# Optimization experiments

Hardware: AMD Instinct MI355X
Metric: run time of the kernel (lower is better)

## Reference

```python
import jax, jax.numpy as jnp
import numpy as np

NUM_Q_HEADS = 32
NUM_KV_GROUPS = 8
HEAD_SIZE = 128
ROPE_THETA = 10000.0


def _rope_cos_sin(T, dim, dtype=jnp.float32):
    # freqs_cis = polar(1, outer(m, 1/theta^(2i/dim)))
    freqs = 1.0 / (ROPE_THETA ** (jnp.arange(0, dim, 2, dtype=jnp.float32) / dim))
    angle = jnp.arange(T, dtype=jnp.float32)[:, None] * freqs[None, :]  # [T, dim/2]
    return jnp.cos(angle).astype(dtype), jnp.sin(angle).astype(dtype)


def _apply_rope(x, cos, sin):
    # x: [B, H, T, D]; adjacent pairs (x[2i], x[2i+1]) form complex numbers
    xr = x[..., 0::2]
    xi = x[..., 1::2]
    or_ = xr * cos - xi * sin
    oi_ = xr * sin + xi * cos
    # interleave back: (..., D/2, 2) -> (..., D)
    out = jnp.stack([or_, oi_], axis=-1)
    return out.reshape(x.shape)


def setup_inputs() -> dict:
    key = jax.random.key(0)
    ks = jax.random.split(key, 5)
    B, T, C = 2, 1024, 4096
    H, G, D = NUM_Q_HEADS, NUM_KV_GROUPS, HEAD_SIZE
    s = 1.0 / np.sqrt(C)
    return {
        "x": jax.random.normal(ks[0], (B, T, C), dtype=jnp.float32),
        "Wq": jax.random.normal(ks[1], (C, H * D), dtype=jnp.float32) * s,
        "Wk": jax.random.normal(ks[2], (C, G * D), dtype=jnp.float32) * s,
        "Wv": jax.random.normal(ks[3], (C, G * D), dtype=jnp.float32) * s,
        "Wo": jax.random.normal(ks[4], (H * D, C), dtype=jnp.float32) * (1.0 / np.sqrt(H * D)),
        "bo": jnp.zeros((C,), dtype=jnp.float32),
    }


def reference(x, Wq, Wk, Wv, Wo, bo):
    B, T, C = x.shape
    H, G, D = NUM_Q_HEADS, NUM_KV_GROUPS, HEAD_SIZE
    rep = H // G

    q = (x @ Wq).reshape(B, T, H, D).transpose(0, 2, 1, 3)  # [B,H,T,D]
    k = (x @ Wk).reshape(B, T, G, D).transpose(0, 2, 1, 3)  # [B,G,T,D]
    v = (x @ Wv).reshape(B, T, G, D).transpose(0, 2, 1, 3)  # [B,G,T,D]

    cos, sin = _rope_cos_sin(T, D)  # [T, D/2]
    q = _apply_rope(q, cos, sin)
    k = _apply_rope(k, cos, sin)

    # GQA: head h uses group h // rep -> reshape instead of repeat_interleave
    qg = q.reshape(B, G, rep, T, D)
    scores = jnp.einsum("bgrtd,bgsd->bgrts", qg, k) * (D ** -0.5)  # [B,G,rep,T,T]

    causal = jnp.tril(jnp.ones((T, T), dtype=bool))
    scores = jnp.where(causal, scores, -jnp.inf)
    probs = jax.nn.softmax(scores, axis=-1)

    out = jnp.einsum("bgrts,bgsd->bgrtd", probs, v)  # [B,G,rep,T,D]
    out = out.reshape(B, H, T, D).transpose(0, 2, 1, 3).reshape(B, T, H * D)
    return out @ Wo + bo
```

## Files before the change

kernel.cpp:

```cpp
#include <hip/hip_runtime.h>
#include <math.h>
#include <cstdint>
#include <cstddef>

typedef __bf16 bf16_t;
typedef __bf16 bf16x8 __attribute__((ext_vector_type(8)));
typedef __bf16 bf16x4 __attribute__((ext_vector_type(4)));
typedef float f32x4 __attribute__((ext_vector_type(4)));
typedef float f32x16 __attribute__((ext_vector_type(16)));

#define MFMA16(a, b, c) __builtin_amdgcn_mfma_f32_16x16x32_bf16(a, b, c, 0, 0, 0)
#define MFMA32(a, b, c) __builtin_amdgcn_mfma_f32_32x32x16_bf16(a, b, c, 0, 0, 0)

__device__ __forceinline__ void stage16(const void* g, void* l) {
  __builtin_amdgcn_global_load_lds(
      (const __attribute__((address_space(1))) unsigned int*)g,
      (__attribute__((address_space(3))) unsigned int*)l, 16, 0, 0);
}

__device__ __forceinline__ bf16x4 shfl_xor32_b64(bf16x4 v) {
  union { bf16x4 h; unsigned int u[2]; } a;
  a.h = v;
  a.u[0] = __shfl_xor(a.u[0], 32);
  a.u[1] = __shfl_xor(a.u[1], 32);
  return a.h;
}

__device__ __forceinline__ bf16x8 cat44(bf16x4 lo, bf16x4 hiv) {
  bf16x8 r;
  r[0] = lo[0]; r[1] = lo[1]; r[2] = lo[2]; r[3] = lo[3];
  r[4] = hiv[0]; r[5] = hiv[1]; r[6] = hiv[2]; r[7] = hiv[3];
  return r;
}

__global__ void k_convert(const float* __restrict__ in, bf16_t* __restrict__ out, int n) {
  int i = (blockIdx.x * blockDim.x + threadIdx.x) * 4;
  if (i >= n) return;
  float4 v = *(const float4*)(in + i);
  out[i + 0] = (bf16_t)v.x;
  out[i + 1] = (bf16_t)v.y;
  out[i + 2] = (bf16_t)v.z;
  out[i + 3] = (bf16_t)v.w;
}

__global__ void k_transpose(const float* __restrict__ in, bf16_t* __restrict__ out,
                            int R, int C) {
  __shared__ float t[32][33];
  int r0 = blockIdx.y * 32, c0 = blockIdx.x * 32;
  int tx = threadIdx.x, ty = threadIdx.y;
#pragma unroll
  for (int i = 0; i < 4; i++)
    t[ty + i * 8][tx] = in[(size_t)(r0 + ty + i * 8) * C + (c0 + tx)];
  __syncthreads();
#pragma unroll
  for (int i = 0; i < 4; i++)
    out[(size_t)(c0 + ty + i * 8) * R + (r0 + tx)] = (bf16_t)t[tx][ty + i * 8];
}

template <int MODE>
__global__ __launch_bounds__(256) void k_gemm(
    const bf16_t* __restrict__ A, const bf16_t* __restrict__ BT,
    float* __restrict__ Cout, const float* __restrict__ bias,
    bf16_t* __restrict__ Qr, bf16_t* __restrict__ Kr, bf16_t* __restrict__ Vt,
    int M, int N, int K) {
  __shared__ __align__(16) bf16_t As[128 * 64];
  __shared__ __align__(16) bf16_t Bs[128 * 64];
  int tid = threadIdx.x;
  int w = tid >> 6, lane = tid & 63, quad = lane >> 4, l16 = lane & 15;
  int n0 = blockIdx.x * 128, m0 = blockIdx.y * 128;
  int wm = (w >> 1) * 64, wn = (w & 1) * 64;
  const char* Ab = (const char*)A + (size_t)m0 * K * 2;
  const char* Bb = (const char*)BT + (size_t)n0 * K * 2;
  size_t rb = (size_t)K * 2;
  f32x4 acc[4][4] = {};
  for (int k0 = 0; k0 < K; k0 += 64) {
    __syncthreads();
#pragma unroll
    for (int it = 0; it < 4; ++it) {
      int P = it * 256 + tid;
      int row = P >> 3, ph = P & 7;
      int c = ph ^ (row & 7);
      stage16(Ab + (size_t)row * rb + (size_t)k0 * 2 + c * 16, (char*)As + P * 16);
      stage16(Bb + (size_t)row * rb + (size_t)k0 * 2 + c * 16, (char*)Bs + P * 16);
    }
    __syncthreads();
#pragma unroll
    for (int ks = 0; ks < 2; ++ks) {
      bf16x8 af[4], bfr[4];
#pragma unroll
      for (int i = 0; i < 4; i++) {
        int row = wm + i * 16 + l16;
        int ph = (ks * 4 + quad) ^ (l16 & 7);
        af[i] = *(const bf16x8*)((const char*)As + row * 128 + ph * 16);
      }
#pragma unroll
      for (int j = 0; j < 4; j++) {
        int row = wn + j * 16 + l16;
        int ph = (ks * 4 + quad) ^ (l16 & 7);
        bfr[j] = *(const bf16x8*)((const char*)Bs + row * 128 + ph * 16);
      }
#pragma unroll
      for (int i = 0; i < 4; i++)
#pragma unroll
        for (int j = 0; j < 4; j++)
          acc[i][j] = MFMA16(af[i], bfr[j], acc[i][j]);
    }
  }

  if (MODE == 0) {
#pragma unroll
    for (int i = 0; i < 4; i++)
#pragma unroll
      for (int j = 0; j < 4; j++) {
        int col = n0 + wn + j * 16 + l16;
        float bv = bias[col];
#pragma unroll
        for (int r = 0; r < 4; r++) {
          int row = m0 + wm + i * 16 + quad * 4 + r;
          Cout[(size_t)row * N + col] = acc[i][j][r] + bv;
        }
      }
  } else {
#pragma unroll
    for (int j = 0; j < 4; j++) {
      int col = n0 + wn + j * 16 + l16;
      if (col < 5120) {
        bf16_t* dst;
        int NH, cb;
        if (col < 4096) { dst = Qr; NH = 32; cb = 0; }
        else            { dst = Kr; NH = 8;  cb = 4096; }
        int cc = col - cb, hh = cc >> 7, d = cc & 127;
#pragma unroll
        for (int i = 0; i < 4; i++)
#pragma unroll
          for (int r = 0; r < 4; r++) {
            int row = m0 + wm + i * 16 + quad * 4 + r;
            int t = row & 1023, bb = row >> 10;
            dst[((size_t)(bb * NH + hh) * 1024 + t) * 128 + d] = (bf16_t)acc[i][j][r];
          }
      } else {
        int gg = (col - 5120) >> 7, d = col & 127;
        int bb = m0 >> 10;
#pragma unroll
        for (int i = 0; i < 4; i++) {
          int t0 = ((m0 + wm + i * 16) & 1023) + quad * 4;
          bf16x4 v4;
#pragma unroll
          for (int r = 0; r < 4; r++) v4[r] = (bf16_t)acc[i][j][r];
          *(bf16x4*)(Vt + ((size_t)(bb * 8 + gg) * 128 + d) * 1024 + t0) = v4;
        }
      }
    }
  }
}

__global__ __launch_bounds__(256) void k_rope(bf16_t* __restrict__ buf, int NH,
                                              float scale) {
  int bt = blockIdx.x;
  int t = bt & 1023, b = bt >> 10;
  int dp = threadIdx.x & 63;
  int h0 = threadIdx.x >> 6;
  float freq = __expf(-(float)dp * (9.210340371976184f / 64.0f));
  float ang = (float)t * freq;
  float sn, cs;
  sincosf(ang, &sn, &cs);
  int hper = NH >> 2;
  for (int i = 0; i < hper; ++i) {
    int h = h0 * hper + i;
    size_t idx = ((size_t)(b * NH + h) * 1024 + t) * 128 + dp * 2;
    float xr = (float)buf[idx], xi = (float)buf[idx + 1];
    buf[idx]     = (bf16_t)((xr * cs - xi * sn) * scale);
    buf[idx + 1] = (bf16_t)((xr * sn + xi * cs) * scale);
  }
}

__global__ __launch_bounds__(256) void k_attn(
    const bf16_t* __restrict__ Q, const bf16_t* __restrict__ K,
    const bf16_t* __restrict__ V, bf16_t* __restrict__ O) {
  __shared__ __align__(16) bf16_t Qs[128 * 128];
  __shared__ __align__(16) bf16_t Ks[64 * 128];
  __shared__ __align__(16) bf16_t Vs[128 * 64];
  int tid = threadIdx.x;
  int w = tid >> 6, lane = tid & 63, hi = lane >> 5, l32 = lane & 31;
  int u = blockIdx.x;
  int rr = u >> 8, s = u & 255;
  int pp0 = s & 7, h = s >> 3, b = rr;
  int tile = rr ? 7 - pp0 : pp0;
  int g = h >> 2;

  const char* Qg = (const char*)Q + ((size_t)(b * 32 + h) * 1024 + tile * 128) * 256;
  const char* Kg = (const char*)K + (size_t)(b * 8 + g) * 1024 * 256;
  const char* Vg = (const char*)V + (size_t)(b * 8 + g) * 128 * 2048;

#pragma unroll
  for (int it = 0; it < 8; ++it) {
    int P = it * 256 + tid;
    int row = P >> 4, ph = P & 15, c = ph ^ (row & 15);
    stage16(Qg + row * 256 + c * 16, (char*)Qs + P * 16);
  }
  __syncthreads();

  bf16x8 qf[8];
#pragma unroll
  for (int kk = 0; kk < 8; ++kk) {
    int row = w * 32 + l32;
    int ph = (kk * 2 + hi) ^ (l32 & 15);
    qf[kk] = *(const bf16x8*)((const char*)Qs + row * 256 + ph * 16);
  }

  f32x16 Oacc[4] = {};
  float m_i = -INFINITY, l_i = 0.0f;
  int q0t = tile * 128 + w * 32;
  int qg = q0t + l32;
  int ktmax = 2 * tile + 1;

  for (int kt = 0; kt <= ktmax; ++kt) {
    int k0 = kt * 64;
    __syncthreads();
#pragma unroll
    for (int it = 0; it < 4; ++it) {
      int P = it * 256 + tid;
      int row = P >> 4, ph = P & 15, c = ph ^ (row & 15);
      stage16(Kg + (size_t)(k0 + row) * 256 + c * 16, (char*)Ks + P * 16);
    }
#pragma unroll
    for (int it = 0; it < 4; ++it) {
      int P = it * 256 + tid;
      int row = P >> 3, ph = P & 7, c = ph ^ (row & 7);
      stage16(Vg + (size_t)row * 2048 + k0 * 2 + c * 16, (char*)Vs + P * 16);
    }
    __syncthreads();
    if (k0 > q0t + 31) continue;

    f32x16 Sa[2];
#pragma unroll
    for (int kt2 = 0; kt2 < 2; ++kt2) {
      f32x16 sacc = {};
#pragma unroll
      for (int kk = 0; kk < 8; ++kk) {
        int row = kt2 * 32 + l32;
        int ph = (kk * 2 + hi) ^ (l32 & 15);
        bf16x8 kf = *(const bf16x8*)((const char*)Ks + row * 256 + ph * 16);
        sacc = MFMA32(kf, qf[kk], sacc);
      }
      Sa[kt2] = sacc;
    }

    float sv[32];
    float mx = -INFINITY;
#pragma unroll
    for (int kt2 = 0; kt2 < 2; ++kt2)
#pragma unroll
      for (int reg = 0; reg < 16; ++reg) {
        float v = Sa[kt2][reg];
        int key = k0 + kt2 * 32 + (reg & 3) + 8 * (reg >> 2) + 4 * hi;
        v = (key <= qg) ? v : -INFINITY;
        sv[kt2 * 16 + reg] = v;
        mx = fmaxf(mx, v);
      }
    mx = fmaxf(mx, __shfl_xor(mx, 32));
    float mn = fmaxf(m_i, mx);
    float alpha = __expf(m_i - mn);
    float sum = 0.0f;
#pragma unroll
    for (int e = 0; e < 32; ++e) {
      float pe = __expf(sv[e] - mn);
      sv[e] = pe;
      sum += pe;
    }
    sum += __shfl_xor(sum, 32);
    m_i = mn;
    l_i = l_i * alpha + sum;

    bf16x8 pf[4];
#pragma unroll
    for (int kt2 = 0; kt2 < 2; ++kt2) {
      bf16x4 pk[4];
#pragma unroll
      for (int gg = 0; gg < 4; ++gg) {
#pragma unroll
        for (int e = 0; e < 4; ++e) pk[gg][e] = (bf16_t)sv[kt2 * 16 + 4 * gg + e];
      }
      bf16x4 X = shfl_xor32_b64(hi ? pk[0] : pk[1]);
      bf16x4 Y = shfl_xor32_b64(hi ? pk[2] : pk[3]);
      pf[2 * kt2]     = (hi == 0) ? cat44(pk[0], X) : cat44(X, pk[1]);
      pf[2 * kt2 + 1] = (hi == 0) ? cat44(pk[2], Y) : cat44(Y, pk[3]);
    }

#pragma unroll
    for (int nt = 0; nt < 4; ++nt) {
      f32x16 o = Oacc[nt];
#pragma unroll
      for (int reg = 0; reg < 16; ++reg) o[reg] *= alpha;
#pragma unroll
      for (int kk = 0; kk < 4; ++kk) {
        int row = nt * 32 + l32;
        int ph = (kk * 2 + hi) ^ (row & 7);
        bf16x8 vf = *(const bf16x8*)((const char*)Vs + row * 128 + ph * 16);
        o = MFMA32(vf, pf[kk], o);
      }
      Oacc[nt] = o;
    }
  }

  float inv = 1.0f / l_i;
  bf16_t* Ob = O + ((size_t)(b * 1024 + qg)) * 4096 + h * 128;
#pragma unroll
  for (int nt = 0; nt < 4; ++nt)
#pragma unroll
    for (int gg = 0; gg < 4; ++gg) {
      bf16x4 o4;
#pragma unroll
      for (int e = 0; e < 4; ++e) o4[e] = (bf16_t)(Oacc[nt][4 * gg + e] * inv);
      *(bf16x4*)(Ob + nt * 32 + 8 * gg + 4 * hi) = o4;
    }
}

extern "C" void kernel_launch(void* const* d_in, const int* in_sizes, int n_in,
                              void* d_out, int out_size, void* d_ws, size_t ws_size,
                              hipStream_t stream) {
  const float* x  = (const float*)d_in[0];
  const float* Wq = (const float*)d_in[1];
  const float* Wk = (const float*)d_in[2];
  const float* Wv = (const float*)d_in[3];
  const float* Wo = (const float*)d_in[4];
  const float* bo = (const float*)d_in[5];
  float* out = (float*)d_out;

  char* p = (char*)d_ws;
  bf16_t* Xb    = (bf16_t*)p; p += (size_t)2048 * 4096 * 2;
  bf16_t* WqkvT = (bf16_t*)p; p += (size_t)6144 * 4096 * 2;
  bf16_t* WoT   = (bf16_t*)p; p += (size_t)4096 * 4096 * 2;
  bf16_t* Qb    = (bf16_t*)p; p += (size_t)2048 * 4096 * 2;
  bf16_t* Kb    = (bf16_t*)p; p += (size_t)2048 * 1024 * 2;
  bf16_t* Vt    = (bf16_t*)p; p += (size_t)2048 * 1024 * 2;
  bf16_t* Ob    = (bf16_t*)p; p += (size_t)2048 * 4096 * 2;

  dim3 tb(32, 8);
  k_convert<<<8192, 256, 0, stream>>>(x, Xb, 2048 * 4096);
  k_transpose<<<dim3(128, 128), tb, 0, stream>>>(Wq, WqkvT, 4096, 4096);
  k_transpose<<<dim3(32, 128),  tb, 0, stream>>>(Wk, WqkvT + (size_t)4096 * 4096, 4096, 1024);
  k_transpose<<<dim3(32, 128),  tb, 0, stream>>>(Wv, WqkvT + (size_t)5120 * 4096, 4096, 1024);
  k_transpose<<<dim3(128, 128), tb, 0, stream>>>(Wo, WoT, 4096, 4096);
  k_gemm<1><<<dim3(48, 16), 256, 0, stream>>>(Xb, WqkvT, nullptr, nullptr,
                                              Qb, Kb, Vt, 2048, 6144, 4096);
  k_rope<<<2048, 256, 0, stream>>>(Qb, 32, 0.08838834764831845f);
  k_rope<<<2048, 256, 0, stream>>>(Kb, 8, 1.0f);
  k_attn<<<512, 256, 0, stream>>>(Qb, Kb, Vt, Ob);
  k_gemm<0><<<dim3(32, 16), 256, 0, stream>>>(Ob, WoT, out, bo,
                                              nullptr, nullptr, nullptr, 2048, 4096, 4096);
}
```

Before: 469.6 us.

## Double-buffer LDS staging in GEMM and attention, use 32x32 MFMA in GEMM

The GEMM now double-buffers its A/B LDS tiles. It prefetches the next K-chunk with global_load_lds while computing the current one, so it needs only one barrier per iteration. It also switches from 16x16x32 to 32x32x16 MFMA tiles, which cuts LDS fragment reads, and its epilogues are rewritten for the new accumulator layout. The attention kernel double-buffers its K/V tiles in one LDS array that reuses the Q staging region. It also skips causal-mask arithmetic on tiles that lie fully below the diagonal. The cost is doubled LDS use in the GEMM, which may lower occupancy, and the extra care needed to avoid buffer aliasing.

```diff
diff --git a/kernel.cpp b/kernel.cpp
--- a/kernel.cpp
+++ b/kernel.cpp
@@ -63,94 +63,106 @@
     float* __restrict__ Cout, const float* __restrict__ bias,
     bf16_t* __restrict__ Qr, bf16_t* __restrict__ Kr, bf16_t* __restrict__ Vt,
     int M, int N, int K) {
-  __shared__ __align__(16) bf16_t As[128 * 64];
-  __shared__ __align__(16) bf16_t Bs[128 * 64];
+  __shared__ __align__(16) bf16_t As[2][128 * 64];
+  __shared__ __align__(16) bf16_t Bs[2][128 * 64];
   int tid = threadIdx.x;
-  int w = tid >> 6, lane = tid & 63, quad = lane >> 4, l16 = lane & 15;
+  int w = tid >> 6, lane = tid & 63, hi = lane >> 5, l32 = lane & 31;
   int n0 = blockIdx.x * 128, m0 = blockIdx.y * 128;
   int wm = (w >> 1) * 64, wn = (w & 1) * 64;
   const char* Ab = (const char*)A + (size_t)m0 * K * 2;
   const char* Bb = (const char*)BT + (size_t)n0 * K * 2;
   size_t rb = (size_t)K * 2;
-  f32x4 acc[4][4] = {};
-  for (int k0 = 0; k0 < K; k0 += 64) {
-    __syncthreads();
+
+  auto stage_chunk = [&](int k0, int buf) {
 #pragma unroll
     for (int it = 0; it < 4; ++it) {
       int P = it * 256 + tid;
       int row = P >> 3, ph = P & 7;
       int c = ph ^ (row & 7);
-      stage16(Ab + (size_t)row * rb + (size_t)k0 * 2 + c * 16, (char*)As + P * 16);
-      stage16(Bb + (size_t)row * rb + (size_t)k0 * 2 + c * 16, (char*)Bs + P * 16);
-    }
+      stage16(Ab + (size_t)row * rb + (size_t)k0 * 2 + c * 16, (char*)As[buf] + P * 16);
+      stage16(Bb + (size_t)row * rb + (size_t)k0 * 2 + c * 16, (char*)Bs[buf] + P * 16);
+    }
+  };
+
+  f32x16 acc[2][2] = {};
+  stage_chunk(0, 0);
+  int nch = K >> 6;
+  for (int cidx = 0; cidx < nch; ++cidx) {
     __syncthreads();
-#pragma unroll
-    for (int ks = 0; ks < 2; ++ks) {
-      bf16x8 af[4], bfr[4];
-#pragma unroll
-      for (int i = 0; i < 4; i++) {
-        int row = wm + i * 16 + l16;
-        int ph = (ks * 4 + quad) ^ (l16 & 7);
-        af[i] = *(const bf16x8*)((const char*)As + row * 128 + ph * 16);
-      }
-#pragma unroll
-      for (int j = 0; j < 4; j++) {
-        int row = wn + j * 16 + l16;
-        int ph = (ks * 4 + quad) ^ (l16 & 7);
-        bfr[j] = *(const bf16x8*)((const char*)Bs + row * 128 + ph * 16);
-      }
-#pragma unroll
-      for (int i = 0; i < 4; i++)
-#pragma unroll
-        for (int j = 0; j < 4; j++)
-          acc[i][j] = MFMA16(af[i], bfr[j], acc[i][j]);
+    if (cidx + 1 < nch) stage_chunk((cidx + 1) << 6, (cidx + 1) & 1);
+    const char* Asb = (const char*)As[cidx & 1];
+    const char* Bsb = (const char*)Bs[cidx & 1];
+#pragma unroll
+    for (int s = 0; s < 4; ++s) {
+      bf16x8 af[2], bfr[2];
+#pragma unroll
+      for (int i = 0; i < 2; ++i) {
+        int row = wm + i * 32 + l32;
+        int ph = (s * 2 + hi) ^ (row & 7);
+        af[i] = *(const bf16x8*)(Asb + row * 128 + ph * 16);
+      }
+#pragma unroll
+      for (int j = 0; j < 2; ++j) {
+        int row = wn + j * 32 + l32;
+        int ph = (s * 2 + hi) ^ (row & 7);
+        bfr[j] = *(const bf16x8*)(Bsb + row * 128 + ph * 16);
+      }
+#pragma unroll
+      for (int i = 0; i < 2; ++i)
+#pragma unroll
+        for (int j = 0; j < 2; ++j)
+          acc[i][j] = MFMA32(af[i], bfr[j], acc[i][j]);
     }
   }
 
   if (MODE == 0) {
 #pragma unroll
-    for (int i = 0; i < 4; i++)
-#pragma unroll
-      for (int j = 0; j < 4; j++) {
-        int col = n0 + wn + j * 16 + l16;
+    for (int i = 0; i < 2; i++)
+#pragma unroll
+      for (int j = 0; j < 2; j++) {
+        int col = n0 + wn + j * 32 + l32;
         float bv = bias[col];
 #pragma unroll
-        for (int r = 0; r < 4; r++) {
-          int row = m0 + wm + i * 16 + quad * 4 + r;
-          Cout[(size_t)row * N + col] = acc[i][j][r] + bv;
+        for (int reg = 0; reg < 16; ++reg) {
+          int row = m0 + wm + i * 32 + (reg & 3) + 8 * (reg >> 2) + 4 * hi;
+          Cout[(size_t)row * N + col] = acc[i][j][reg] + bv;
         }
       }
+  } else if (n0 < 5120) {
+    bf16_t* dst;
+    int NH, cb;
+    if (n0 < 4096) { dst = Qr; NH = 32; cb = 0; }
+    else           { dst = Kr; NH = 8;  cb = 4096; }
+#pragma unroll
+    for (int i = 0; i < 2; i++)
+#pragma unroll
+      for (int j = 0; j < 2; j++) {
+        int cc = (n0 - cb) + wn + j * 32 + l32;
+        int hh = cc >> 7, d = cc & 127;
+#pragma unroll
+        for (int reg = 0; reg < 16; ++reg) {
+          int row = m0 + wm + i * 32 + (reg & 3) + 8 * (reg >> 2) + 4 * hi;
+          int t = row & 1023, bb = row >> 10;
+          dst[((size_t)(bb * NH + hh) * 1024 + t) * 128 + d] = (bf16_t)acc[i][j][reg];
+        }
+      }
   } else {
-#pragma unroll
-    for (int j = 0; j < 4; j++) {
-      int col = n0 + wn + j * 16 + l16;
-      if (col < 5120) {
-        bf16_t* dst;
-        int NH, cb;
-        if (col < 4096) { dst = Qr; NH = 32; cb = 0; }
-        else            { dst = Kr; NH = 8;  cb = 4096; }
-        int cc = col - cb, hh = cc >> 7, d = cc & 127;
-#pragma unroll
-        for (int i = 0; i < 4; i++)
-#pragma unroll
-          for (int r = 0; r < 4; r++) {
-            int row = m0 + wm + i * 16 + quad * 4 + r;
-            int t = row & 1023, bb = row >> 10;
-            dst[((size_t)(bb * NH + hh) * 1024 + t) * 128 + d] = (bf16_t)acc[i][j][r];
-          }
-      } else {
-        int gg = (col - 5120) >> 7, d = col & 127;
-        int bb = m0 >> 10;
-#pragma unroll
-        for (int i = 0; i < 4; i++) {
-          int t0 = ((m0 + wm + i * 16) & 1023) + quad * 4;
+    int bb = m0 >> 10;
+#pragma unroll
+    for (int i = 0; i < 2; i++)
+#pragma unroll
+      for (int j = 0; j < 2; j++) {
+        int cc = (n0 - 5120) + wn + j * 32 + l32;
+        int gg = cc >> 7, d = cc & 127;
+#pragma unroll
+        for (int rg = 0; rg < 4; ++rg) {
+          int t0 = ((m0 + wm + i * 32) & 1023) + 8 * rg + 4 * hi;
           bf16x4 v4;
 #pragma unroll
-          for (int r = 0; r < 4; r++) v4[r] = (bf16_t)acc[i][j][r];
+          for (int e = 0; e < 4; ++e) v4[e] = (bf16_t)acc[i][j][rg * 4 + e];
           *(bf16x4*)(Vt + ((size_t)(bb * 8 + gg) * 128 + d) * 1024 + t0) = v4;
         }
       }
-    }
   }
 }
 
@@ -177,9 +189,8 @@
 __global__ __launch_bounds__(256) void k_attn(
     const bf16_t* __restrict__ Q, const bf16_t* __restrict__ K,
     const bf16_t* __restrict__ V, bf16_t* __restrict__ O) {
-  __shared__ __align__(16) bf16_t Qs[128 * 128];
-  __shared__ __align__(16) bf16_t Ks[64 * 128];
-  __shared__ __align__(16) bf16_t Vs[128 * 64];
+  __shared__ __align__(16) bf16_t lds[32768];
+  bf16_t* Qs = lds + 16384;
   int tid = threadIdx.x;
   int w = tid >> 6, lane = tid & 63, hi = lane >> 5, l32 = lane & 31;
   int u = blockIdx.x;
@@ -208,29 +219,37 @@
     qf[kk] = *(const bf16x8*)((const char*)Qs + row * 256 + ph * 16);
   }
 
+  auto stageKV = [&](int k0, int buf) {
+    char* Kb_ = (char*)(lds + buf * 16384);
+    char* Vb_ = (char*)(lds + buf * 16384 + 8192);
+#pragma unroll
+    for (int it = 0; it < 4; ++it) {
+      int P = it * 256 + tid;
+      int row = P >> 4, ph = P & 15, c = ph ^ (row & 15);
+      stage16(Kg + (size_t)(k0 + row) * 256 + c * 16, Kb_ + P * 16);
+    }
+#pragma unroll
+    for (int it = 0; it < 4; ++it) {
+      int P = it * 256 + tid;
+      int row = P >> 3, ph = P & 7, c = ph ^ (row & 7);
+      stage16(Vg + (size_t)row * 2048 + (size_t)k0 * 2 + c * 16, Vb_ + P * 16);
+    }
+  };
+
   f32x16 Oacc[4] = {};
   float m_i = -INFINITY, l_i = 0.0f;
   int q0t = tile * 128 + w * 32;
   int qg = q0t + l32;
   int ktmax = 2 * tile + 1;
 
+  stageKV(0, 0);
   for (int kt = 0; kt <= ktmax; ++kt) {
     int k0 = kt * 64;
     __syncthreads();
-#pragma unroll
-    for (int it = 0; it < 4; ++it) {
-      int P = it * 256 + tid;
-      int row = P >> 4, ph = P & 15, c = ph ^ (row & 15);
-      stage16(Kg + (size_t)(k0 + row) * 256 + c * 16, (char*)Ks + P * 16);
-    }
-#pragma unroll
-    for (int it = 0; it < 4; ++it) {
-      int P = it * 256 + tid;
-      int row = P >> 3, ph = P & 7, c = ph ^ (row & 7);
-      stage16(Vg + (size_t)row * 2048 + k0 * 2 + c * 16, (char*)Vs + P * 16);
-    }
-    __syncthreads();
+    if (kt < ktmax) stageKV(k0 + 64, (kt + 1) & 1);
     if (k0 > q0t + 31) continue;
+    const char* Ksb = (const char*)(lds + (kt & 1) * 16384);
+    const char* Vsb = (const char*)(lds + (kt & 1) * 16384 + 8192);
 
     f32x16 Sa[2];
 #pragma unroll
@@ -240,12 +259,13 @@
       for (int kk = 0; kk < 8; ++kk) {
         int row = kt2 * 32 + l32;
         int ph = (kk * 2 + hi) ^ (l32 & 15);
-        bf16x8 kf = *(const bf16x8*)((const char*)Ks + row * 256 + ph * 16);
+        bf16x8 kf = *(const bf16x8*)(Ksb + row * 256 + ph * 16);
         sacc = MFMA32(kf, qf[kk], sacc);
       }
       Sa[kt2] = sacc;
     }
 
+    bool needmask = (k0 + 63) > q0t;
     float sv[32];
     float mx = -INFINITY;
 #pragma unroll
@@ -253,8 +273,10 @@
 #pragma unroll
       for (int reg = 0; reg < 16; ++reg) {
         float v = Sa[kt2][reg];
-        int key = k0 + kt2 * 32 + (reg & 3) + 8 * (reg >> 2) + 4 * hi;
-        v = (key <= qg) ? v : -INFINITY;
+        if (needmask) {
+          int key = k0 + kt2 * 32 + (reg & 3) + 8 * (reg >> 2) + 4 * hi;
+          v = (key <= qg) ? v : -INFINITY;
+        }
         sv[kt2 * 16 + reg] = v;
         mx = fmaxf(mx, v);
       }
@@ -296,7 +318,7 @@
       for (int kk = 0; kk < 4; ++kk) {
         int row = nt * 32 + l32;
         int ph = (kk * 2 + hi) ^ (row & 7);
-        bf16x8 vf = *(const bf16x8*)((const char*)Vs + row * 128 + ph * 16);
+        bf16x8 vf = *(const bf16x8*)(Vsb + row * 128 + ph * 16);
         o = MFMA32(vf, pf[kk], o);
       }
       Oacc[nt] = o;
```

Result: slower. 518.1 us (+10.3%).
